# Optimization experiments

Hardware: AMD Instinct MI355X
Metric: run time of the kernel (lower is better)

Reference implementation:

```python
import jax, jax.numpy as jnp
import numpy as np

K = 4
C = 512
CLAMP = (1e-4, 1.0 - 1e-4)
INIT_ALPHAS = (0.8, 0.9, 0.98, 0.99)


def setup_inputs() -> dict:
    key = jax.random.key(0)
    kx, = jax.random.split(key, 1)
    B, T = 16, 4096
    x = jax.random.normal(kx, (B, T, C), dtype=jnp.float32)
    # logit_alpha: [K, C], each row initialized to logit(alpha_k)
    alphas = np.clip(np.array(INIT_ALPHAS[:K], dtype=np.float32), CLAMP[0], CLAMP[1])
    logit = np.log(alphas / (1.0 - alphas))  # logit
    logit_alpha = jnp.asarray(np.repeat(logit[:, None], C, axis=1), dtype=jnp.float32)
    mix_logits = jnp.zeros((C, K), dtype=jnp.float32)
    return {"x": x, "logit_alpha": logit_alpha, "mix_logits": mix_logits}


def reference(x, logit_alpha, mix_logits):
    # x: [B, T, C]; logit_alpha: [K, C]; mix_logits: [C, K]
    B, T, Cc = x.shape
    x32 = x.astype(jnp.float32)
    a = jnp.clip(jax.nn.sigmoid(logit_alpha.astype(jnp.float32)), CLAMP[0], CLAMP[1])  # [K, C]
    one_minus_a = 1.0 - a

    y0 = jnp.broadcast_to(x32[:, 0, None, :], (B, K, Cc))  # [B, K, C]

    def step(y_prev, xt):  # y_prev: [B,K,C], xt: [B,C]
        y = a * y_prev + one_minus_a * xt[:, None, :]
        return y, y

    xs = jnp.swapaxes(x32[:, 1:, :], 0, 1)  # [T-1, B, C]
    _, ys = jax.lax.scan(step, y0, xs)  # ys: [T-1, B, K, C]
    yk_all = jnp.concatenate([y0[None], ys], axis=0)  # [T, B, K, C]

    mix = jax.nn.softmax(mix_logits.astype(jnp.float32), axis=-1)  # [C, K]
    trend = jnp.einsum('tbkc,ck->btc', yk_all, mix)
    return trend.astype(x.dtype)
```

## Files before the change

### kernel.cpp

```cpp
#include <hip/hip_runtime.h>

#define B_  16
#define T_  4096
#define C_  512
#define K_  4
#define NT_ 64
#define L_  (T_ / NT_)

__device__ __forceinline__ float sigmoid_clamp(float la) {
    float av = 1.0f / (1.0f + expf(-la));
    return fminf(fmaxf(av, 1e-4f), 1.0f - 1e-4f);
}

__global__ __launch_bounds__(512) void ema_pass1(const float* __restrict__ x,
                                                 const float* __restrict__ logit_alpha,
                                                 float* __restrict__ ws) {
    const int c = threadIdx.x;
    const int b = blockIdx.x / NT_;
    const int j = blockIdx.x % NT_;

    float a[K_], oma[K_], s[K_];
#pragma unroll
    for (int k = 0; k < K_; ++k) {
        float av = sigmoid_clamp(logit_alpha[k * C_ + c]);
        a[k] = av; oma[k] = 1.0f - av; s[k] = 0.0f;
    }

    const float* xp = x + ((size_t)b * T_ + (size_t)j * L_) * C_ + c;
#pragma unroll 4
    for (int i = 0; i < L_; ++i) {
        float xv = xp[(size_t)i * C_];
#pragma unroll
        for (int k = 0; k < K_; ++k)
            s[k] = fmaf(a[k], s[k], oma[k] * xv);
    }

#pragma unroll
    for (int k = 0; k < K_; ++k)
        ws[(((size_t)b * K_ + k) * NT_ + j) * C_ + c] = s[k];
}

__global__ __launch_bounds__(512) void ema_pass2(const float* __restrict__ x,
                                                 const float* __restrict__ logit_alpha,
                                                 float* __restrict__ ws) {
    const int c = threadIdx.x;
    const int b = blockIdx.x / K_;
    const int k = blockIdx.x % K_;

    float av = sigmoid_clamp(logit_alpha[k * C_ + c]);
    float A = av;
#pragma unroll
    for (int q = 0; q < 6; ++q) A *= A;

    float carry = x[(size_t)b * T_ * C_ + c];
    float* wsb = ws + ((size_t)b * K_ + k) * NT_ * C_ + c;
    for (int j = 0; j < NT_; ++j) {
        float sj = wsb[(size_t)j * C_];
        wsb[(size_t)j * C_] = carry;
        carry = fmaf(A, carry, sj);
    }
}

__global__ __launch_bounds__(512) void ema_pass3(const float* __restrict__ x,
                                                 const float* __restrict__ logit_alpha,
                                                 const float* __restrict__ mix_logits,
                                                 const float* __restrict__ ws,
                                                 float* __restrict__ out) {
    const int c = threadIdx.x;
    const int b = blockIdx.x / NT_;
    const int j = blockIdx.x % NT_;

    float a[K_], oma[K_], y[K_], m[K_];
#pragma unroll
    for (int k = 0; k < K_; ++k) {
        float av = sigmoid_clamp(logit_alpha[k * C_ + c]);
        a[k] = av; oma[k] = 1.0f - av;
        y[k] = ws[(((size_t)b * K_ + k) * NT_ + j) * C_ + c];
    }

    float mx = -INFINITY;
#pragma unroll
    for (int k = 0; k < K_; ++k) { m[k] = mix_logits[(size_t)c * K_ + k]; mx = fmaxf(mx, m[k]); }
    float den = 0.0f;
#pragma unroll
    for (int k = 0; k < K_; ++k) { m[k] = expf(m[k] - mx); den += m[k]; }
    float inv = 1.0f / den;
#pragma unroll
    for (int k = 0; k < K_; ++k) m[k] *= inv;

    const float* xp = x + ((size_t)b * T_ + (size_t)j * L_) * C_ + c;
    float*       op = out + ((size_t)b * T_ + (size_t)j * L_) * C_ + c;
#pragma unroll 4
    for (int i = 0; i < L_; ++i) {
        float xv = xp[(size_t)i * C_];
        float acc = 0.0f;
#pragma unroll
        for (int k = 0; k < K_; ++k) {
            y[k] = fmaf(a[k], y[k], oma[k] * xv);
            acc = fmaf(m[k], y[k], acc);
        }
        op[(size_t)i * C_] = acc;
    }
}

extern "C" void kernel_launch(void* const* d_in, const int* in_sizes, int n_in,
                              void* d_out, int out_size, void* d_ws, size_t ws_size,
                              hipStream_t stream) {
    const float* x           = (const float*)d_in[0];
    const float* logit_alpha = (const float*)d_in[1];
    const float* mix_logits  = (const float*)d_in[2];
    float* out = (float*)d_out;
    float* ws  = (float*)d_ws;

    ema_pass1<<<B_ * NT_, 512, 0, stream>>>(x, logit_alpha, ws);
    ema_pass2<<<B_ * K_,  512, 0, stream>>>(x, logit_alpha, ws);
    ema_pass3<<<B_ * NT_, 512, 0, stream>>>(x, logit_alpha, mix_logits, ws, out);
}
```

Baseline: 72.98 us.

## Vectorize EMA passes with float4 loads, nontemporal stores, and finer pass2 grid

Passes 1 and 3 now have each thread handle four channels through float4 loads and stores, with two time chunks per 256-thread block. Pass 3 writes its output with nontemporal stores. Pass 2 is split into 128-thread blocks per channel quarter, giving four times as many blocks to raise parallelism in the serial carry scan. The goal is wider memory transactions and fewer instructions per byte, at the cost of fewer total threads in passes 1 and 3, which may reduce latency hiding.

```diff
diff --git a/kernel.cpp b/kernel.cpp
--- a/kernel.cpp
+++ b/kernel.cpp
@@ -6,46 +6,60 @@
 #define K_  4
 #define NT_ 64
 #define L_  (T_ / NT_)
+#define C4_ (C_ / 4)
+
+typedef float nfloat4 __attribute__((ext_vector_type(4)));
 
 __device__ __forceinline__ float sigmoid_clamp(float la) {
     float av = 1.0f / (1.0f + expf(-la));
     return fminf(fmaxf(av, 1e-4f), 1.0f - 1e-4f);
 }
 
-__global__ __launch_bounds__(512) void ema_pass1(const float* __restrict__ x,
+__global__ __launch_bounds__(256) void ema_pass1(const float4* __restrict__ x4,
                                                  const float* __restrict__ logit_alpha,
-                                                 float* __restrict__ ws) {
-    const int c = threadIdx.x;
-    const int b = blockIdx.x / NT_;
-    const int j = blockIdx.x % NT_;
+                                                 float4* __restrict__ ws4) {
+    const int c4 = threadIdx.x & (C4_ - 1);
+    const int jh = threadIdx.x >> 7;
+    const int b  = blockIdx.x / (NT_ / 2);
+    const int j  = (blockIdx.x % (NT_ / 2)) * 2 + jh;
 
-    float a[K_], oma[K_], s[K_];
+    float4 a[K_], oma[K_], s[K_];
 #pragma unroll
     for (int k = 0; k < K_; ++k) {
-        float av = sigmoid_clamp(logit_alpha[k * C_ + c]);
-        a[k] = av; oma[k] = 1.0f - av; s[k] = 0.0f;
+        float4 la = ((const float4*)logit_alpha)[k * C4_ + c4];
+        a[k].x = sigmoid_clamp(la.x); a[k].y = sigmoid_clamp(la.y);
+        a[k].z = sigmoid_clamp(la.z); a[k].w = sigmoid_clamp(la.w);
+        oma[k].x = 1.0f - a[k].x; oma[k].y = 1.0f - a[k].y;
+        oma[k].z = 1.0f - a[k].z; oma[k].w = 1.0f - a[k].w;
+        s[k].x = s[k].y = s[k].z = s[k].w = 0.0f;
     }
 
-    const float* xp = x + ((size_t)b * T_ + (size_t)j * L_) * C_ + c;
+    const float4* xp = x4 + ((size_t)b * T_ + (size_t)j * L_) * C4_ + c4;
 #pragma unroll 4
     for (int i = 0; i < L_; ++i) {
-        float xv = xp[(size_t)i * C_];
+        float4 xv = xp[(size_t)i * C4_];
 #pragma unroll
-        for (int k = 0; k < K_; ++k)
-            s[k] = fmaf(a[k], s[k], oma[k] * xv);
+        for (int k = 0; k < K_; ++k) {
+            s[k].x = fmaf(a[k].x, s[k].x, oma[k].x * xv.x);
+            s[k].y = fmaf(a[k].y, s[k].y, oma[k].y * xv.y);
+            s[k].z = fmaf(a[k].z, s[k].z, oma[k].z * xv.z);
+            s[k].w = fmaf(a[k].w, s[k].w, oma[k].w * xv.w);
+        }
     }
 
 #pragma unroll
     for (int k = 0; k < K_; ++k)
-        ws[(((size_t)b * K_ + k) * NT_ + j) * C_ + c] = s[k];
+        ws4[(((size_t)b * K_ + k) * NT_ + j) * C4_ + c4] = s[k];
 }
 
-__global__ __launch_bounds__(512) void ema_pass2(const float* __restrict__ x,
+__global__ __launch_bounds__(128) void ema_pass2(const float* __restrict__ x,
                                                  const float* __restrict__ logit_alpha,
                                                  float* __restrict__ ws) {
-    const int c = threadIdx.x;
-    const int b = blockIdx.x / K_;
-    const int k = blockIdx.x % K_;
+    const int ct = blockIdx.x & 3;
+    const int bk = blockIdx.x >> 2;
+    const int b  = bk / K_;
+    const int k  = bk % K_;
+    const int c  = ct * 128 + threadIdx.x;
 
     float av = sigmoid_clamp(logit_alpha[k * C_ + c]);
     float A = av;
@@ -61,45 +75,58 @@
     }
 }
 
-__global__ __launch_bounds__(512) void ema_pass3(const float* __restrict__ x,
+__global__ __launch_bounds__(256) void ema_pass3(const float4* __restrict__ x4,
                                                  const float* __restrict__ logit_alpha,
-                                                 const float* __restrict__ mix_logits,
-                                                 const float* __restrict__ ws,
-                                                 float* __restrict__ out) {
-    const int c = threadIdx.x;
-    const int b = blockIdx.x / NT_;
-    const int j = blockIdx.x % NT_;
+                                                 const float4* __restrict__ ml4,
+                                                 const float4* __restrict__ ws4,
+                                                 float4* __restrict__ out4) {
+    const int c4 = threadIdx.x & (C4_ - 1);
+    const int jh = threadIdx.x >> 7;
+    const int b  = blockIdx.x / (NT_ / 2);
+    const int j  = (blockIdx.x % (NT_ / 2)) * 2 + jh;
 
-    float a[K_], oma[K_], y[K_], m[K_];
+    float4 a[K_], oma[K_], y[K_];
+    float  m[K_][4];
 #pragma unroll
     for (int k = 0; k < K_; ++k) {
-        float av = sigmoid_clamp(logit_alpha[k * C_ + c]);
-        a[k] = av; oma[k] = 1.0f - av;
-        y[k] = ws[(((size_t)b * K_ + k) * NT_ + j) * C_ + c];
+        float4 la = ((const float4*)logit_alpha)[k * C4_ + c4];
+        a[k].x = sigmoid_clamp(la.x); a[k].y = sigmoid_clamp(la.y);
+        a[k].z = sigmoid_clamp(la.z); a[k].w = sigmoid_clamp(la.w);
+        oma[k].x = 1.0f - a[k].x; oma[k].y = 1.0f - a[k].y;
+        oma[k].z = 1.0f - a[k].z; oma[k].w = 1.0f - a[k].w;
+        y[k] = ws4[(((size_t)b * K_ + k) * NT_ + j) * C4_ + c4];
     }
 
-    float mx = -INFINITY;
 #pragma unroll
-    for (int k = 0; k < K_; ++k) { m[k] = mix_logits[(size_t)c * K_ + k]; mx = fmaxf(mx, m[k]); }
-    float den = 0.0f;
-#pragma unroll
-    for (int k = 0; k < K_; ++k) { m[k] = expf(m[k] - mx); den += m[k]; }
-    float inv = 1.0f / den;
-#pragma unroll
-    for (int k = 0; k < K_; ++k) m[k] *= inv;
+    for (int ci = 0; ci < 4; ++ci) {
+        float4 ml = ml4[(size_t)c4 * 4 + ci];
+        float mx = fmaxf(fmaxf(ml.x, ml.y), fmaxf(ml.z, ml.w));
+        float e0 = expf(ml.x - mx), e1 = expf(ml.y - mx);
+        float e2 = expf(ml.z - mx), e3 = expf(ml.w - mx);
+        float inv = 1.0f / (e0 + e1 + e2 + e3);
+        m[0][ci] = e0 * inv; m[1][ci] = e1 * inv;
+        m[2][ci] = e2 * inv; m[3][ci] = e3 * inv;
+    }
 
-    const float* xp = x + ((size_t)b * T_ + (size_t)j * L_) * C_ + c;
-    float*       op = out + ((size_t)b * T_ + (size_t)j * L_) * C_ + c;
+    const float4* xp = x4   + ((size_t)b * T_ + (size_t)j * L_) * C4_ + c4;
+    float4*       op = out4 + ((size_t)b * T_ + (size_t)j * L_) * C4_ + c4;
 #pragma unroll 4
     for (int i = 0; i < L_; ++i) {
-        float xv = xp[(size_t)i * C_];
-        float acc = 0.0f;
+        float4 xv = xp[(size_t)i * C4_];
+        float4 acc; acc.x = acc.y = acc.z = acc.w = 0.0f;
 #pragma unroll
         for (int k = 0; k < K_; ++k) {
-            y[k] = fmaf(a[k], y[k], oma[k] * xv);
-            acc = fmaf(m[k], y[k], acc);
+            y[k].x = fmaf(a[k].x, y[k].x, oma[k].x * xv.x);
+            y[k].y = fmaf(a[k].y, y[k].y, oma[k].y * xv.y);
+            y[k].z = fmaf(a[k].z, y[k].z, oma[k].z * xv.z);
+            y[k].w = fmaf(a[k].w, y[k].w, oma[k].w * xv.w);
+            acc.x = fmaf(m[k][0], y[k].x, acc.x);
+            acc.y = fmaf(m[k][1], y[k].y, acc.y);
+            acc.z = fmaf(m[k][2], y[k].z, acc.z);
+            acc.w = fmaf(m[k][3], y[k].w, acc.w);
         }
-        op[(size_t)i * C_] = acc;
+        nfloat4 nv = { acc.x, acc.y, acc.z, acc.w };
+        __builtin_nontemporal_store(nv, (nfloat4*)&op[(size_t)i * C4_]);
     }
 }
 
@@ -112,7 +139,10 @@
     float* out = (float*)d_out;
     float* ws  = (float*)d_ws;
 
-    ema_pass1<<<B_ * NT_, 512, 0, stream>>>(x, logit_alpha, ws);
-    ema_pass2<<<B_ * K_,  512, 0, stream>>>(x, logit_alpha, ws);
-    ema_pass3<<<B_ * NT_, 512, 0, stream>>>(x, logit_alpha, mix_logits, ws, out);
+    ema_pass1<<<B_ * NT_ / 2, 256, 0, stream>>>((const float4*)x, logit_alpha,
+                                                (float4*)ws);
+    ema_pass2<<<B_ * K_ * 4, 128, 0, stream>>>(x, logit_alpha, ws);
+    ema_pass3<<<B_ * NT_ / 2, 256, 0, stream>>>((const float4*)x, logit_alpha,
+                                                (const float4*)mix_logits,
+                                                (const float4*)ws, (float4*)out);
 }
```

Measured after the change: 75.71 us. +3.7%, slower.
